# Kernel optimization log

Measured on AMD Instinct MI355X. Metric: run time of the kernel, lower is better.

## Reference

```python
import jax, jax.numpy as jnp
import numpy as np
from jax import lax

HEADS = 4
SR = 4
LN_EPS = 1e-5


def setup_inputs() -> dict:
    key = jax.random.key(0)
    ks = jax.random.split(key, 8)
    B, N, C = 8, 4096, 256
    w_scale = 0.05  # keep attention logits in a sane range
    return {
        "x": jax.random.normal(ks[0], (B, N, C), jnp.float32),
        "h": 64,
        "w": 64,
        "Wq": jax.random.normal(ks[1], (C, C), jnp.float32) * w_scale,
        "Wkv": jax.random.normal(ks[2], (C, 2 * C), jnp.float32) * w_scale,
        "sr_w": jax.random.normal(ks[3], (C, C, SR, SR), jnp.float32) * w_scale,
        "sr_b": jnp.zeros((C,), jnp.float32),
        "ln_g": jnp.ones((C,), jnp.float32),
        "ln_b": jnp.zeros((C,), jnp.float32),
        "Wo": jax.random.normal(ks[4], (C, C), jnp.float32) * w_scale,
        "bo": jnp.zeros((C,), jnp.float32),
    }


def _layernorm(x, g, b):
    mu = x.mean(-1, keepdims=True)
    var = ((x - mu) ** 2).mean(-1, keepdims=True)
    return (x - mu) * lax.rsqrt(var + LN_EPS) * g + b


def reference(x, h, w, Wq, Wkv, sr_w, sr_b, ln_g, ln_b, Wo, bo):
    B, N, C = x.shape
    hd = C // HEADS
    scale = hd ** -0.5
    # Q projection -> [B, H, N, hd]
    q = (x @ Wq).reshape(B, N, HEADS, hd).transpose(0, 2, 1, 3)
    # spatial reduction of K/V tokens: strided conv + LayerNorm
    x_kv = x.transpose(0, 2, 1).reshape(B, C, h, w)  # b (h w) c -> b c h w
    x_kv = lax.conv_general_dilated(
        x_kv, sr_w, window_strides=(SR, SR), padding="VALID",
        dimension_numbers=("NCHW", "OIHW", "NCHW"))
    x_kv = x_kv + sr_b[None, :, None, None]
    Nk = (h // SR) * (w // SR)
    x_kv = x_kv.reshape(B, C, Nk).transpose(0, 2, 1)  # b c h w -> b (h w) c
    x_kv = _layernorm(x_kv, ln_g, ln_b)
    # KV projection -> k, v each [B, H, Nk, hd]
    kv = (x_kv @ Wkv).reshape(B, Nk, 2, HEADS, hd)
    k = kv[:, :, 0].transpose(0, 2, 1, 3)
    v = kv[:, :, 1].transpose(0, 2, 1, 3)
    # attention: full [B, H, N, Nk] score matrix, softmax over kv axis
    att = jax.nn.softmax(jnp.einsum("bhxd,bhyd->bhxy", q, k) * scale, axis=-1)
    out = jnp.einsum("bhxy,bhyd->bhxd", att, v)
    out = out.transpose(0, 2, 1, 3).reshape(B, N, C)  # b h l d -> b l (h d)
    return out @ Wo + bo
```

## Files before the change

kernel.cpp:

```cpp
#include <hip/hip_runtime.h>

typedef __bf16 bf16;
typedef bf16 bf16x8 __attribute__((ext_vector_type(8)));
typedef bf16 bf16x4 __attribute__((ext_vector_type(4)));
typedef float f32x4 __attribute__((ext_vector_type(4)));

#define MFMA16(a, b, c) __builtin_amdgcn_mfma_f32_16x16x32_bf16(a, b, c, 0, 0, 0)

__device__ __forceinline__ void gload_lds16(const bf16* g, bf16* l) {
  __builtin_amdgcn_global_load_lds(
      (const __attribute__((address_space(1))) void*)g,
      (__attribute__((address_space(3))) void*)l, 16, 0, 0);
}

__global__ void k_prep(const float* __restrict__ x, const float* __restrict__ Wq,
                       const float* __restrict__ Wkv, const float* __restrict__ Wo,
                       const float* __restrict__ srw,
                       bf16* __restrict__ x_bf, bf16* __restrict__ WqT,
                       bf16* __restrict__ WkvT, bf16* __restrict__ WoT,
                       bf16* __restrict__ srwT) {
  int bid = blockIdx.x, tid = threadIdx.x;
  if (bid < 8192) {
    int i = (bid * 256 + tid) * 4;
    float4 v = *(const float4*)(x + i);
    bf16x4 o;
    o[0] = (bf16)v.x; o[1] = (bf16)v.y; o[2] = (bf16)v.z; o[3] = (bf16)v.w;
    *(bf16x4*)(x_bf + i) = o;
  } else if (bid < 9216) {
    int id = (bid - 8192) * 256 + tid;
    if (id < 65536) {
      int c = id >> 8, r = id & 255;
      WqT[c * 256 + (r ^ ((c & 7) << 3))] = (bf16)Wq[r * 256 + c];
    } else if (id < 196608) {
      int l = id - 65536;
      int c = l >> 8, r = l & 255;
      WkvT[l] = (bf16)Wkv[r * 512 + c];
    } else {
      int l = id - 196608;
      int c = l >> 8, r = l & 255;
      WoT[l] = (bf16)Wo[r * 256 + c];
    }
  } else {
    int id4 = ((bid - 9216) * 256 + tid) * 4;
    int o = id4 >> 12, rem = id4 & 4095;
    int i = rem >> 4, p = rem & 15;
    float4 v = *(const float4*)(srw + id4);
    srwT[(o << 12) + ((p + 0) << 8) + i] = (bf16)v.x;
    srwT[(o << 12) + ((p + 1) << 8) + i] = (bf16)v.y;
    srwT[(o << 12) + ((p + 2) << 8) + i] = (bf16)v.z;
    srwT[(o << 12) + ((p + 3) << 8) + i] = (bf16)v.w;
  }
}

template <int AMODE, int EMODE>
__global__ __launch_bounds__(256, 2) void k_gemm(
    const bf16* __restrict__ A, const bf16* __restrict__ Bt,
    void* __restrict__ Cout, const float* __restrict__ bias,
    int M, int N, int K) {
  constexpr int LDT = 72;
  __shared__ alignas(16) bf16 As[64 * LDT];
  __shared__ alignas(16) bf16 Bs[64 * LDT];
  int tid = threadIdx.x;
  int m0 = blockIdx.x * 64, n0 = blockIdx.y * 64;
  int kbeg = blockIdx.z * K;
  int wave = tid >> 6, lane = tid & 63;
  int quad = lane >> 4, l16 = lane & 15;

  f32x4 acc[4];
#pragma unroll
  for (int i = 0; i < 4; i++) acc[i] = (f32x4){0.f, 0.f, 0.f, 0.f};

  for (int k0 = kbeg; k0 < kbeg + K; k0 += 64) {
#pragma unroll
    for (int t = 0; t < 2; t++) {
      int c = tid + t * 256;
      int row = c >> 3, c8 = (c & 7) * 8;
      *(bf16x8*)&As[row * LDT + c8] =
          *(const bf16x8*)(A + (size_t)(m0 + row) * K + k0 + c8);
      *(bf16x8*)&Bs[row * LDT + c8] =
          *(const bf16x8*)(Bt + (size_t)(n0 + row) * K + k0 + c8);
    }
    __syncthreads();
#pragma unroll
    for (int kk = 0; kk < 64; kk += 32) {
      bf16x8 af = *(const bf16x8*)&As[(wave * 16 + l16) * LDT + kk + quad * 8];
#pragma unroll
      for (int nt = 0; nt < 4; nt++) {
        bf16x8 bfr = *(const bf16x8*)&Bs[(nt * 16 + l16) * LDT + kk + quad * 8];
        acc[nt] = MFMA16(af, bfr, acc[nt]);
      }
    }
    __syncthreads();
  }

  int rbase = m0 + wave * 16 + quad * 4;
#pragma unroll
  for (int nt = 0; nt < 4; nt++) {
    int col = n0 + nt * 16 + l16;
#pragma unroll
    for (int r = 0; r < 4; r++) {
      float v = acc[nt][r];
      int row = rbase + r;
      if constexpr (EMODE == 2) {
        int b = row >> 8, key = row & 255;
        int isv = col >> 8, c2 = col & 255;
        int hh = c2 >> 6, d = c2 & 63;
        int bh = b * 4 + hh;
        bf16* dst = (bf16*)Cout;
        if (isv == 0)
          dst[(((size_t)bh) * 256 + key) * 64 + (d ^ ((key & 7) << 3))] = (bf16)v;
        else
          dst[32 * 256 * 64 + (((size_t)bh) * 64 + d) * 256 + (key ^ ((d & 7) << 3))] = (bf16)v;
      } else {
        ((float*)Cout)[(size_t)row * N + col] = v + bias[col];
      }
    }
  }
}

template <int AMODE, int EMODE>
__global__ __launch_bounds__(256, 2) void k_gemm128(
    const bf16* __restrict__ A, const bf16* __restrict__ Bt,
    void* __restrict__ Cout, const float* __restrict__ bias,
    int M, int N, int K) {
  __shared__ alignas(16) bf16 As[128 * 64];
  __shared__ alignas(16) bf16 Bs[128 * 64];
  int tid = threadIdx.x;
  int m0 = blockIdx.x * 128, n0 = blockIdx.y * 128;
  int kbeg = blockIdx.z * K;
  int wave = tid >> 6, lane = tid & 63;
  int quad = lane >> 4, l16 = lane & 15;
  int wr = wave >> 1, wc = wave & 1;

  f32x4 acc[4][4];
#pragma unroll
  for (int i = 0; i < 4; i++)
#pragma unroll
    for (int j = 0; j < 4; j++) acc[i][j] = (f32x4){0.f, 0.f, 0.f, 0.f};

  for (int k0 = kbeg; k0 < kbeg + K; k0 += 64) {
#pragma unroll
    for (int t = 0; t < 4; t++) {
      int chunk = wave * 4 + t;
      int row = chunk * 8 + (lane >> 3);
      int c8 = (lane & 7) * 8;
      const bf16* asrc;
      if constexpr (AMODE == 0) {
        asrc = A + (size_t)(m0 + row) * K + k0 + c8;
      } else {
        int m = m0 + row;
        int b = m >> 8, tt = m & 255;
        int oh = tt >> 4, ow = tt & 15;
        int p = k0 >> 8;
        int kh = p >> 2, kw = p & 3;
        int tok = (oh * 4 + kh) * 64 + ow * 4 + kw;
        asrc = A + ((size_t)(b * 4096 + tok) << 8) + (k0 & 255) + c8;
      }
      gload_lds16(asrc, As + chunk * 512);
      gload_lds16(Bt + (size_t)(n0 + row) * ((AMODE == 1) ? 4096 : K) + k0 + c8,
                  Bs + chunk * 512);
    }
    __syncthreads();
#pragma unroll
    for (int kk = 0; kk < 64; kk += 32) {
      bf16x8 af[4], bfr[4];
#pragma unroll
      for (int mt = 0; mt < 4; mt++)
        af[mt] = *(const bf16x8*)&As[(wr * 64 + mt * 16 + l16) * 64 + kk + quad * 8];
#pragma unroll
      for (int nt = 0; nt < 4; nt++)
        bfr[nt] = *(const bf16x8*)&Bs[(wc * 64 + nt * 16 + l16) * 64 + kk + quad * 8];
#pragma unroll
      for (int mt = 0; mt < 4; mt++)
#pragma unroll
        for (int nt = 0; nt < 4; nt++)
          acc[mt][nt] = MFMA16(af[mt], bfr[nt], acc[mt][nt]);
    }
    __syncthreads();
  }

#pragma unroll
  for (int mt = 0; mt < 4; mt++) {
    int rbase = m0 + wr * 64 + mt * 16 + quad * 4;
#pragma unroll
    for (int nt = 0; nt < 4; nt++) {
      int col = n0 + wc * 64 + nt * 16 + l16;
#pragma unroll
      for (int r = 0; r < 4; r++) {
        float v = acc[mt][nt][r];
        int row = rbase + r;
        if constexpr (EMODE == 3) {
          ((float*)Cout)[(size_t)row * N + col] = v + bias[col];
        } else {
          ((float*)Cout)[((size_t)blockIdx.z * M + row) * N + col] = v;
        }
      }
    }
  }
}

__global__ void k_ln(const float* __restrict__ part, const float* __restrict__ srb,
                     const float* __restrict__ g, const float* __restrict__ bb,
                     bf16* __restrict__ out) {
  int row = blockIdx.x * 4 + (threadIdx.x >> 6);
  int lane = threadIdx.x & 63;
  size_t off = (size_t)row * 256 + lane * 4;
  float4 v = *(const float4*)&part[off];
#pragma unroll
  for (int z = 1; z < 8; z++) {
    float4 p = *(const float4*)&part[(size_t)z * 2048 * 256 + off];
    v.x += p.x; v.y += p.y; v.z += p.z; v.w += p.w;
  }
  int c = lane * 4;
  v.x += srb[c + 0]; v.y += srb[c + 1]; v.z += srb[c + 2]; v.w += srb[c + 3];
  float s = v.x + v.y + v.z + v.w;
#pragma unroll
  for (int i = 1; i < 64; i <<= 1) s += __shfl_xor(s, i, 64);
  float mu = s * (1.f / 256.f);
  float d0 = v.x - mu, d1 = v.y - mu, d2 = v.z - mu, d3 = v.w - mu;
  float q = d0 * d0 + d1 * d1 + d2 * d2 + d3 * d3;
#pragma unroll
  for (int i = 1; i < 64; i <<= 1) q += __shfl_xor(q, i, 64);
  float rs = rsqrtf(q * (1.f / 256.f) + 1e-5f);
  bf16x4 o;
  o[0] = (bf16)(d0 * rs * g[c + 0] + bb[c + 0]);
  o[1] = (bf16)(d1 * rs * g[c + 1] + bb[c + 1]);
  o[2] = (bf16)(d2 * rs * g[c + 2] + bb[c + 2]);
  o[3] = (bf16)(d3 * rs * g[c + 3] + bb[c + 3]);
  *(bf16x4*)&out[(size_t)row * 256 + c] = o;
}

__global__ __launch_bounds__(256, 3) void k_attn(
    const bf16* __restrict__ xbf,
    const bf16* __restrict__ WqT,
    const bf16* __restrict__ Kg,
    const bf16* __restrict__ Vg,
    bf16* __restrict__ O) {
  int bh = blockIdx.x, qt = blockIdx.y;
  int b = bh >> 2, h = bh & 3;
  int tid = threadIdx.x, wave = tid >> 6, lane = tid & 63;
  int quad = lane >> 4, l16 = lane & 15;

  __shared__ alignas(16) bf16 smem[24576];
  bf16* R0  = smem;
  bf16* R2a = smem + 16384;
  bf16* R2b = smem + 20480;

  const bf16* Kbh = Kg + ((size_t)bh << 14);
  const bf16* Vbh = Vg + ((size_t)bh << 14);
  const bf16* Wqh = WqT + ((size_t)(h * 64) << 8);

#pragma unroll
  for (int t = 0; t < 8; t++) {
    int chunk = t * 4 + wave;
    gload_lds16(Wqh + chunk * 512 + lane * 8, R0 + chunk * 512);
  }
#pragma unroll
  for (int t = 0; t < 2; t++) {
    int chunk = wave * 2 + t;
    gload_lds16(Vbh + (chunk * 8 + (lane >> 3)) * 256 + 0 + (lane & 7) * 8,
                R2a + chunk * 512);
  }
  const bf16* xrow =
      xbf + (((size_t)(b * 4096 + qt * 64 + wave * 16 + l16)) << 8) + quad * 8;
  bf16x8 ax[8];
#pragma unroll
  for (int j = 0; j < 8; j++) ax[j] = *(const bf16x8*)(xrow + j * 32);

  __syncthreads();

  f32x4 q[4];
#pragma unroll
  for (int i = 0; i < 4; i++) q[i] = (f32x4){0.f, 0.f, 0.f, 0.f};
#pragma unroll
  for (int j = 0; j < 8; j++) {
#pragma unroll
    for (int nt = 0; nt < 4; nt++) {
      int wrow = nt * 16 + l16;
      bf16x8 bw = *(const bf16x8*)&R0[wrow * 256 +
                                      ((j * 32 + quad * 8) ^ ((wrow & 7) << 3))];
      q[nt] = MFMA16(ax[j], bw, q[nt]);
    }
  }
  __syncthreads();

#pragma unroll
  for (int nt = 0; nt < 4; nt++)
#pragma unroll
    for (int r = 0; r < 4; r++) {
      int qr = wave * 16 + quad * 4 + r;
      R2b[qr * 64 + ((nt * 16 + l16) ^ ((qr & 7) << 3))] = (bf16)q[nt][r];
    }
#pragma unroll
  for (int t = 0; t < 8; t++) {
    int chunk = t * 4 + wave;
    gload_lds16(Kbh + chunk * 512 + lane * 8, R0 + chunk * 512);
  }
  __syncthreads();

  int arow = wave * 16 + l16;
  int asw = (arow & 7) << 3;
  bf16x8 aq0 = *(const bf16x8*)&R2b[arow * 64 + ((quad * 8) ^ asw)];
  bf16x8 aq1 = *(const bf16x8*)&R2b[arow * 64 + ((32 + quad * 8) ^ asw)];
  asm volatile("s_waitcnt lgkmcnt(0)" ::: "memory");
#pragma unroll
  for (int t = 0; t < 2; t++) {
    int chunk = wave * 2 + t;
    gload_lds16(Vbh + (chunk * 8 + (lane >> 3)) * 256 + 64 + (lane & 7) * 8,
                R2b + chunk * 512);
  }

  f32x4 s[16];
#pragma unroll
  for (int i = 0; i < 16; i++) s[i] = (f32x4){0.f, 0.f, 0.f, 0.f};
#pragma unroll
  for (int nt = 0; nt < 16; nt++) {
    int krow = nt * 16 + l16;
    const bf16* kb = R0 + krow * 64;
    int sw = (krow & 7) << 3;
    bf16x8 b0 = *(const bf16x8*)(kb + ((quad * 8) ^ sw));
    bf16x8 b1 = *(const bf16x8*)(kb + ((32 + quad * 8) ^ sw));
    s[nt] = MFMA16(aq0, b0, s[nt]);
    s[nt] = MFMA16(aq1, b1, s[nt]);
  }

  const float scale = 0.125f;
#pragma unroll
  for (int r = 0; r < 4; r++) {
    float m = -1e30f;
#pragma unroll
    for (int nt = 0; nt < 16; nt++) m = fmaxf(m, s[nt][r]);
#pragma unroll
    for (int i = 1; i < 16; i <<= 1) m = fmaxf(m, __shfl_xor(m, i, 64));
    float sum = 0.f;
#pragma unroll
    for (int nt = 0; nt < 16; nt++) {
      float e = __expf((s[nt][r] - m) * scale);
      s[nt][r] = e;
      sum += e;
    }
#pragma unroll
    for (int i = 1; i < 16; i <<= 1) sum += __shfl_xor(sum, i, 64);
    float inv = 1.f / sum;
#pragma unroll
    for (int nt = 0; nt < 16; nt++) s[nt][r] *= inv;
  }

  __syncthreads();

#pragma unroll
  for (int nt = 0; nt < 16; nt++)
#pragma unroll
    for (int r = 0; r < 4; r++) {
      int prow = wave * 16 + quad * 4 + r;
      R0[prow * 256 + ((nt * 16 + l16) ^ ((prow & 7) << 3))] = (bf16)s[nt][r];
    }

  const bf16* pb = R0 + arow * 256;
  f32x4 o[4];
#pragma unroll
  for (int i = 0; i < 4; i++) o[i] = (f32x4){0.f, 0.f, 0.f, 0.f};

#pragma unroll
  for (int cq = 0; cq < 4; cq++) {
    const bf16* Vbuf = (cq & 1) ? R2b : R2a;
#pragma unroll
    for (int k0 = 0; k0 < 64; k0 += 32) {
      bf16x8 ap = *(const bf16x8*)(pb + ((cq * 64 + k0 + quad * 8) ^ asw));
#pragma unroll
      for (int nt = 0; nt < 4; nt++) {
        int vrow = nt * 16 + l16;
        bf16x8 bv = *(const bf16x8*)&Vbuf[vrow * 64 +
                                          ((k0 + quad * 8) ^ ((vrow & 7) << 3))];
        o[nt] = MFMA16(ap, bv, o[nt]);
      }
    }
    if (cq < 3) {
      __syncthreads();
      if (cq < 2) {
        bf16* nb = (cq & 1) ? R2b : R2a;
#pragma unroll
        for (int t = 0; t < 2; t++) {
          int chunk = wave * 2 + t;
          gload_lds16(Vbh + (chunk * 8 + (lane >> 3)) * 256 + (cq + 2) * 64 +
                          (lane & 7) * 8,
                      nb + chunk * 512);
        }
      }
    }
  }

  size_t orow = (size_t)b * 4096 + qt * 64 + wave * 16 + quad * 4;
#pragma unroll
  for (int nt = 0; nt < 4; nt++) {
    int col = h * 64 + nt * 16 + l16;
#pragma unroll
    for (int r = 0; r < 4; r++) O[(orow + r) * 256 + col] = (bf16)o[nt][r];
  }
}

extern "C" void kernel_launch(void* const* d_in, const int* in_sizes, int n_in,
                              void* d_out, int out_size, void* d_ws, size_t ws_size,
                              hipStream_t stream) {
  (void)in_sizes; (void)n_in; (void)out_size; (void)ws_size;
  const float* x   = (const float*)d_in[0];
  const float* Wq  = (const float*)d_in[3];
  const float* Wkv = (const float*)d_in[4];
  const float* srw = (const float*)d_in[5];
  const float* srb = (const float*)d_in[6];
  const float* lng = (const float*)d_in[7];
  const float* lnb = (const float*)d_in[8];
  const float* Wo  = (const float*)d_in[9];
  const float* bo  = (const float*)d_in[10];
  float* out = (float*)d_out;

  char* ws = (char*)d_ws;
  bf16*  x_bf  = (bf16*)(ws + 0);
  bf16*  AObuf = (bf16*)(ws + 16777216);
  float* convp = (float*)(ws + 33554432);
  bf16*  WqT   = (bf16*)(ws + 50331648);
  bf16*  WkvT  = (bf16*)(ws + 50462720);
  bf16*  WoT   = (bf16*)(ws + 50724864);
  bf16*  srwT  = (bf16*)(ws + 50855936);
  bf16*  xln   = (bf16*)(ws + 52953088);
  bf16*  kvbuf = (bf16*)(ws + 54001664);

  k_prep<<<10240, 256, 0, stream>>>(x, Wq, Wkv, Wo, srw, x_bf, WqT, WkvT, WoT, srwT);
  k_gemm128<1, 4><<<dim3(16, 2, 8), 256, 0, stream>>>(x_bf, srwT, convp, nullptr, 2048, 256, 512);
  k_ln<<<512, 256, 0, stream>>>(convp, srb, lng, lnb, xln);
  k_gemm<0, 2><<<dim3(32, 8), 256, 0, stream>>>(xln, WkvT, kvbuf, nullptr, 2048, 512, 256);
  k_attn<<<dim3(32, 64), 256, 0, stream>>>(x_bf, WqT, kvbuf, kvbuf + (size_t)32 * 256 * 64, AObuf);
  k_gemm128<0, 3><<<dim3(256, 2), 256, 0, stream>>>(AObuf, WoT, out, bo, 32768, 256, 256);
}
```

Measured before the change: 177.0 us.

## Fuse output projection into attention kernel and loop over all heads per block

Each attention block now processes one 64-row query tile across all four heads, keeping per-head outputs in registers. It then applies the Wo projection and bias in-kernel, writing fp32 output directly. This removes the bf16 intermediate attention-output buffer round trip and the separate output GEMM launch. Wo is pre-swizzled in prep to match the LDS layout. The trade-off is that the grid drops from 2048 to 512 blocks, each doing serialized per-head work with more barriers, lower occupancy (launch bound 3 to 2) and higher register pressure.

```diff
diff --git a/kernel.cpp b/kernel.cpp
--- a/kernel.cpp
+++ b/kernel.cpp
@@ -38,7 +38,7 @@
     } else {
       int l = id - 196608;
       int c = l >> 8, r = l & 255;
-      WoT[l] = (bf16)Wo[r * 256 + c];
+      WoT[c * 256 + (r ^ ((c & 7) << 3))] = (bf16)Wo[r * 256 + c];
     }
   } else {
     int id4 = ((bid - 9216) * 256 + tid) * 4;
@@ -230,172 +230,196 @@
   *(bf16x4*)&out[(size_t)row * 256 + c] = o;
 }
 
-__global__ __launch_bounds__(256, 3) void k_attn(
+__global__ __launch_bounds__(256, 2) void k_attn_mega(
     const bf16* __restrict__ xbf,
     const bf16* __restrict__ WqT,
     const bf16* __restrict__ Kg,
     const bf16* __restrict__ Vg,
-    bf16* __restrict__ O) {
-  int bh = blockIdx.x, qt = blockIdx.y;
-  int b = bh >> 2, h = bh & 3;
+    const bf16* __restrict__ WoT,
+    const float* __restrict__ bo,
+    float* __restrict__ out) {
+  int b = blockIdx.x, qt = blockIdx.y;
   int tid = threadIdx.x, wave = tid >> 6, lane = tid & 63;
   int quad = lane >> 4, l16 = lane & 15;
 
-  __shared__ alignas(16) bf16 smem[24576];
-  bf16* R0  = smem;
-  bf16* R2a = smem + 16384;
-  bf16* R2b = smem + 20480;
-
-  const bf16* Kbh = Kg + ((size_t)bh << 14);
-  const bf16* Vbh = Vg + ((size_t)bh << 14);
-  const bf16* Wqh = WqT + ((size_t)(h * 64) << 8);
-
-#pragma unroll
-  for (int t = 0; t < 8; t++) {
-    int chunk = t * 4 + wave;
-    gload_lds16(Wqh + chunk * 512 + lane * 8, R0 + chunk * 512);
-  }
-#pragma unroll
-  for (int t = 0; t < 2; t++) {
-    int chunk = wave * 2 + t;
-    gload_lds16(Vbh + (chunk * 8 + (lane >> 3)) * 256 + 0 + (lane & 7) * 8,
-                R2a + chunk * 512);
-  }
-  const bf16* xrow =
-      xbf + (((size_t)(b * 4096 + qt * 64 + wave * 16 + l16)) << 8) + quad * 8;
-  bf16x8 ax[8];
-#pragma unroll
-  for (int j = 0; j < 8; j++) ax[j] = *(const bf16x8*)(xrow + j * 32);
-
-  __syncthreads();
-
-  f32x4 q[4];
-#pragma unroll
-  for (int i = 0; i < 4; i++) q[i] = (f32x4){0.f, 0.f, 0.f, 0.f};
-#pragma unroll
-  for (int j = 0; j < 8; j++) {
-#pragma unroll
-    for (int nt = 0; nt < 4; nt++) {
-      int wrow = nt * 16 + l16;
-      bf16x8 bw = *(const bf16x8*)&R0[wrow * 256 +
-                                      ((j * 32 + quad * 8) ^ ((wrow & 7) << 3))];
-      q[nt] = MFMA16(ax[j], bw, q[nt]);
-    }
-  }
-  __syncthreads();
-
-#pragma unroll
-  for (int nt = 0; nt < 4; nt++)
-#pragma unroll
-    for (int r = 0; r < 4; r++) {
-      int qr = wave * 16 + quad * 4 + r;
-      R2b[qr * 64 + ((nt * 16 + l16) ^ ((qr & 7) << 3))] = (bf16)q[nt][r];
-    }
-#pragma unroll
-  for (int t = 0; t < 8; t++) {
-    int chunk = t * 4 + wave;
-    gload_lds16(Kbh + chunk * 512 + lane * 8, R0 + chunk * 512);
-  }
-  __syncthreads();
+  __shared__ alignas(16) bf16 smem[36864];
+  bf16* R0 = smem;
+  bf16* RV = smem + 16384;
+  bf16* RQ = smem + 32768;
 
   int arow = wave * 16 + l16;
   int asw = (arow & 7) << 3;
-  bf16x8 aq0 = *(const bf16x8*)&R2b[arow * 64 + ((quad * 8) ^ asw)];
-  bf16x8 aq1 = *(const bf16x8*)&R2b[arow * 64 + ((32 + quad * 8) ^ asw)];
-  asm volatile("s_waitcnt lgkmcnt(0)" ::: "memory");
-#pragma unroll
-  for (int t = 0; t < 2; t++) {
-    int chunk = wave * 2 + t;
-    gload_lds16(Vbh + (chunk * 8 + (lane >> 3)) * 256 + 64 + (lane & 7) * 8,
-                R2b + chunk * 512);
-  }
-
-  f32x4 s[16];
-#pragma unroll
-  for (int i = 0; i < 16; i++) s[i] = (f32x4){0.f, 0.f, 0.f, 0.f};
-#pragma unroll
-  for (int nt = 0; nt < 16; nt++) {
-    int krow = nt * 16 + l16;
-    const bf16* kb = R0 + krow * 64;
-    int sw = (krow & 7) << 3;
-    bf16x8 b0 = *(const bf16x8*)(kb + ((quad * 8) ^ sw));
-    bf16x8 b1 = *(const bf16x8*)(kb + ((32 + quad * 8) ^ sw));
-    s[nt] = MFMA16(aq0, b0, s[nt]);
-    s[nt] = MFMA16(aq1, b1, s[nt]);
-  }
-
-  const float scale = 0.125f;
-#pragma unroll
-  for (int r = 0; r < 4; r++) {
-    float m = -1e30f;
-#pragma unroll
-    for (int nt = 0; nt < 16; nt++) m = fmaxf(m, s[nt][r]);
-#pragma unroll
-    for (int i = 1; i < 16; i <<= 1) m = fmaxf(m, __shfl_xor(m, i, 64));
-    float sum = 0.f;
+
+  const bf16* xrow =
+      xbf + (((size_t)(b * 4096 + qt * 64 + arow)) << 8) + quad * 8;
+  bf16x8 ax[8];
+#pragma unroll
+  for (int j = 0; j < 8; j++) ax[j] = *(const bf16x8*)(xrow + j * 32);
+
+  f32x4 o_all[4][4];
+
+#pragma unroll
+  for (int h = 0; h < 4; h++) {
+    int bh = b * 4 + h;
+    const bf16* Wqh = WqT + ((size_t)(h * 64) << 8);
+    const bf16* Kbh = Kg + ((size_t)bh << 14);
+    const bf16* Vbh = Vg + ((size_t)bh << 14);
+
+#pragma unroll
+    for (int t = 0; t < 8; t++) {
+      int chunk = t * 4 + wave;
+      gload_lds16(Wqh + chunk * 512 + lane * 8, R0 + chunk * 512);
+    }
+    __syncthreads();
+
+#pragma unroll
+    for (int t = 0; t < 8; t++) {
+      int chunk = t * 4 + wave;
+      gload_lds16(Vbh + chunk * 512 + lane * 8, RV + chunk * 512);
+    }
+
+    f32x4 q[4];
+#pragma unroll
+    for (int i = 0; i < 4; i++) q[i] = (f32x4){0.f, 0.f, 0.f, 0.f};
+#pragma unroll
+    for (int j = 0; j < 8; j++) {
+#pragma unroll
+      for (int nt = 0; nt < 4; nt++) {
+        int wrow = nt * 16 + l16;
+        bf16x8 bw = *(const bf16x8*)&R0[wrow * 256 +
+                                        ((j * 32 + quad * 8) ^ ((wrow & 7) << 3))];
+        q[nt] = MFMA16(ax[j], bw, q[nt]);
+      }
+    }
+    __syncthreads();
+
+#pragma unroll
+    for (int nt = 0; nt < 4; nt++)
+#pragma unroll
+      for (int r = 0; r < 4; r++) {
+        int qr = wave * 16 + quad * 4 + r;
+        RQ[qr * 64 + ((nt * 16 + l16) ^ ((qr & 7) << 3))] = (bf16)q[nt][r];
+      }
+#pragma unroll
+    for (int t = 0; t < 8; t++) {
+      int chunk = t * 4 + wave;
+      gload_lds16(Kbh + chunk * 512 + lane * 8, R0 + chunk * 512);
+    }
+    __syncthreads();
+
+    bf16x8 aq0 = *(const bf16x8*)&RQ[arow * 64 + ((quad * 8) ^ asw)];
+    bf16x8 aq1 = *(const bf16x8*)&RQ[arow * 64 + ((32 + quad * 8) ^ asw)];
+
+    f32x4 s[16];
+#pragma unroll
+    for (int i = 0; i < 16; i++) s[i] = (f32x4){0.f, 0.f, 0.f, 0.f};
 #pragma unroll
     for (int nt = 0; nt < 16; nt++) {
-      float e = __expf((s[nt][r] - m) * scale);
-      s[nt][r] = e;
-      sum += e;
-    }
-#pragma unroll
-    for (int i = 1; i < 16; i <<= 1) sum += __shfl_xor(sum, i, 64);
-    float inv = 1.f / sum;
-#pragma unroll
-    for (int nt = 0; nt < 16; nt++) s[nt][r] *= inv;
-  }
-
-  __syncthreads();
-
-#pragma unroll
-  for (int nt = 0; nt < 16; nt++)
+      int krow = nt * 16 + l16;
+      const bf16* kb = R0 + krow * 64;
+      int sw = (krow & 7) << 3;
+      bf16x8 b0 = *(const bf16x8*)(kb + ((quad * 8) ^ sw));
+      bf16x8 b1 = *(const bf16x8*)(kb + ((32 + quad * 8) ^ sw));
+      s[nt] = MFMA16(aq0, b0, s[nt]);
+      s[nt] = MFMA16(aq1, b1, s[nt]);
+    }
+
+    const float scale = 0.125f;
 #pragma unroll
     for (int r = 0; r < 4; r++) {
-      int prow = wave * 16 + quad * 4 + r;
-      R0[prow * 256 + ((nt * 16 + l16) ^ ((prow & 7) << 3))] = (bf16)s[nt][r];
-    }
-
-  const bf16* pb = R0 + arow * 256;
-  f32x4 o[4];
-#pragma unroll
-  for (int i = 0; i < 4; i++) o[i] = (f32x4){0.f, 0.f, 0.f, 0.f};
-
-#pragma unroll
-  for (int cq = 0; cq < 4; cq++) {
-    const bf16* Vbuf = (cq & 1) ? R2b : R2a;
-#pragma unroll
-    for (int k0 = 0; k0 < 64; k0 += 32) {
-      bf16x8 ap = *(const bf16x8*)(pb + ((cq * 64 + k0 + quad * 8) ^ asw));
+      float m = -1e30f;
+#pragma unroll
+      for (int nt = 0; nt < 16; nt++) m = fmaxf(m, s[nt][r]);
+#pragma unroll
+      for (int i = 1; i < 16; i <<= 1) m = fmaxf(m, __shfl_xor(m, i, 64));
+      float sum = 0.f;
+#pragma unroll
+      for (int nt = 0; nt < 16; nt++) {
+        float e = __expf((s[nt][r] - m) * scale);
+        s[nt][r] = e;
+        sum += e;
+      }
+#pragma unroll
+      for (int i = 1; i < 16; i <<= 1) sum += __shfl_xor(sum, i, 64);
+      float inv = 1.f / sum;
+#pragma unroll
+      for (int nt = 0; nt < 16; nt++) s[nt][r] *= inv;
+    }
+
+    __syncthreads();
+
+#pragma unroll
+    for (int nt = 0; nt < 16; nt++)
+#pragma unroll
+      for (int r = 0; r < 4; r++) {
+        int prow = wave * 16 + quad * 4 + r;
+        R0[prow * 256 + ((nt * 16 + l16) ^ ((prow & 7) << 3))] = (bf16)s[nt][r];
+      }
+
+    const bf16* pb = R0 + arow * 256;
+#pragma unroll
+    for (int nt = 0; nt < 4; nt++) o_all[h][nt] = (f32x4){0.f, 0.f, 0.f, 0.f};
+#pragma unroll
+    for (int k0 = 0; k0 < 256; k0 += 32) {
+      bf16x8 ap = *(const bf16x8*)(pb + ((k0 + quad * 8) ^ asw));
 #pragma unroll
       for (int nt = 0; nt < 4; nt++) {
         int vrow = nt * 16 + l16;
-        bf16x8 bv = *(const bf16x8*)&Vbuf[vrow * 64 +
-                                          ((k0 + quad * 8) ^ ((vrow & 7) << 3))];
-        o[nt] = MFMA16(ap, bv, o[nt]);
-      }
-    }
-    if (cq < 3) {
-      __syncthreads();
-      if (cq < 2) {
-        bf16* nb = (cq & 1) ? R2b : R2a;
-#pragma unroll
-        for (int t = 0; t < 2; t++) {
-          int chunk = wave * 2 + t;
-          gload_lds16(Vbh + (chunk * 8 + (lane >> 3)) * 256 + (cq + 2) * 64 +
-                          (lane & 7) * 8,
-                      nb + chunk * 512);
-        }
-      }
-    }
-  }
-
-  size_t orow = (size_t)b * 4096 + qt * 64 + wave * 16 + quad * 4;
-#pragma unroll
-  for (int nt = 0; nt < 4; nt++) {
-    int col = h * 64 + nt * 16 + l16;
-#pragma unroll
-    for (int r = 0; r < 4; r++) O[(orow + r) * 256 + col] = (bf16)o[nt][r];
+        bf16x8 bv = *(const bf16x8*)&RV[vrow * 256 +
+                                        ((k0 + quad * 8) ^ ((vrow & 7) << 3))];
+        o_all[h][nt] = MFMA16(ap, bv, o_all[h][nt]);
+      }
+    }
+    __syncthreads();
+  }
+
+#pragma unroll
+  for (int h = 0; h < 4; h++)
+#pragma unroll
+    for (int nt = 0; nt < 4; nt++)
+#pragma unroll
+      for (int r = 0; r < 4; r++) {
+        int orow = wave * 16 + quad * 4 + r;
+        int col = h * 64 + nt * 16 + l16;
+        R0[orow * 256 + (col ^ ((orow & 7) << 3))] = (bf16)o_all[h][nt][r];
+      }
+  bf16x8 oa[8];
+#pragma unroll
+  for (int j = 0; j < 8; j++)
+    oa[j] = *(const bf16x8*)&R0[arow * 256 + ((j * 32 + quad * 8) ^ asw)];
+
+  size_t orow0 = (size_t)b * 4096 + qt * 64 + wave * 16 + quad * 4;
+#pragma unroll
+  for (int c = 0; c < 4; c++) {
+#pragma unroll
+    for (int t = 0; t < 8; t++) {
+      int chunk = t * 4 + wave;
+      gload_lds16(WoT + (((size_t)c * 64) << 8) + chunk * 512 + lane * 8,
+                  RV + chunk * 512);
+    }
+    __syncthreads();
+
+    f32x4 oo[4];
+#pragma unroll
+    for (int i = 0; i < 4; i++) oo[i] = (f32x4){0.f, 0.f, 0.f, 0.f};
+#pragma unroll
+    for (int j = 0; j < 8; j++) {
+#pragma unroll
+      for (int nt = 0; nt < 4; nt++) {
+        int wrow = nt * 16 + l16;
+        bf16x8 bw = *(const bf16x8*)&RV[wrow * 256 +
+                                        ((j * 32 + quad * 8) ^ ((wrow & 7) << 3))];
+        oo[nt] = MFMA16(oa[j], bw, oo[nt]);
+      }
+    }
+#pragma unroll
+    for (int nt = 0; nt < 4; nt++) {
+      int col = c * 64 + nt * 16 + l16;
+#pragma unroll
+      for (int r = 0; r < 4; r++)
+        out[(orow0 + r) * 256 + col] = oo[nt][r] + bo[col];
+    }
+    if (c < 3) __syncthreads();
   }
 }
 
@@ -416,19 +440,18 @@
 
   char* ws = (char*)d_ws;
   bf16*  x_bf  = (bf16*)(ws + 0);
-  bf16*  AObuf = (bf16*)(ws + 16777216);
-  float* convp = (float*)(ws + 33554432);
-  bf16*  WqT   = (bf16*)(ws + 50331648);
-  bf16*  WkvT  = (bf16*)(ws + 50462720);
-  bf16*  WoT   = (bf16*)(ws + 50724864);
-  bf16*  srwT  = (bf16*)(ws + 50855936);
-  bf16*  xln   = (bf16*)(ws + 52953088);
-  bf16*  kvbuf = (bf16*)(ws + 54001664);
+  float* convp = (float*)(ws + 16777216);
+  bf16*  WqT   = (bf16*)(ws + 33554432);
+  bf16*  WkvT  = (bf16*)(ws + 33685504);
+  bf16*  WoT   = (bf16*)(ws + 33947648);
+  bf16*  srwT  = (bf16*)(ws + 34078720);
+  bf16*  xln   = (bf16*)(ws + 36175872);
+  bf16*  kvbuf = (bf16*)(ws + 37224448);
 
   k_prep<<<10240, 256, 0, stream>>>(x, Wq, Wkv, Wo, srw, x_bf, WqT, WkvT, WoT, srwT);
   k_gemm128<1, 4><<<dim3(16, 2, 8), 256, 0, stream>>>(x_bf, srwT, convp, nullptr, 2048, 256, 512);
   k_ln<<<512, 256, 0, stream>>>(convp, srb, lng, lnb, xln);
   k_gemm<0, 2><<<dim3(32, 8), 256, 0, stream>>>(xln, WkvT, kvbuf, nullptr, 2048, 512, 256);
-  k_attn<<<dim3(32, 64), 256, 0, stream>>>(x_bf, WqT, kvbuf, kvbuf + (size_t)32 * 256 * 64, AObuf);
-  k_gemm128<0, 3><<<dim3(256, 2), 256, 0, stream>>>(AObuf, WoT, out, bo, 32768, 256, 256);
-}
+  k_attn_mega<<<dim3(8, 64), 256, 0, stream>>>(
+      x_bf, WqT, kvbuf, kvbuf + (size_t)32 * 256 * 64, WoT, bo, out);
+}
```

After: 180.5 us. No clear change (+2.0%).

## Add dedicated 64-row output projection GEMM and raise MFMA priority in attention

Applied to the files above, without the earlier changes.

Replaces the generic 128-tile output projection GEMM with a specialized kernel where each block computes 64 rows by the full 256 output columns. Each wave owns 64 columns and the A tile is shared by all waves, giving 512 blocks for better CU fill, with the bias add fused into the store. It also wraps the MFMA loops in the attention kernel with s_setprio so waves issuing matrix math get scheduling priority over waves doing loads. The new GEMM uses unswizzled LDS reads and reloads the full 256-row weight tile in every block, which may cause bank conflicts and extra memory traffic.

```diff
diff --git a/kernel.cpp b/kernel.cpp
--- a/kernel.cpp
+++ b/kernel.cpp
@@ -199,6 +199,69 @@
   }
 }
 
+__global__ __launch_bounds__(256, 3) void k_gemm_out(
+    const bf16* __restrict__ A, const bf16* __restrict__ Bt,
+    float* __restrict__ out, const float* __restrict__ bias) {
+  __shared__ alignas(16) bf16 As[64 * 64];
+  __shared__ alignas(16) bf16 Bs[256 * 64];
+  int tid = threadIdx.x;
+  int m0 = blockIdx.x * 64;
+  int wave = tid >> 6, lane = tid & 63;
+  int quad = lane >> 4, l16 = lane & 15;
+
+  f32x4 acc[4][4];
+#pragma unroll
+  for (int i = 0; i < 4; i++)
+#pragma unroll
+    for (int j = 0; j < 4; j++) acc[i][j] = (f32x4){0.f, 0.f, 0.f, 0.f};
+
+  for (int k0 = 0; k0 < 256; k0 += 64) {
+    int c8 = (lane & 7) * 8;
+#pragma unroll
+    for (int t = 0; t < 2; t++) {
+      int chunk = wave * 2 + t;
+      int row = chunk * 8 + (lane >> 3);
+      gload_lds16(A + (size_t)(m0 + row) * 256 + k0 + c8, As + chunk * 512);
+    }
+#pragma unroll
+    for (int t = 0; t < 8; t++) {
+      int chunk = wave * 8 + t;
+      int row = chunk * 8 + (lane >> 3);
+      gload_lds16(Bt + (size_t)row * 256 + k0 + c8, Bs + chunk * 512);
+    }
+    __syncthreads();
+#pragma unroll
+    for (int kk = 0; kk < 64; kk += 32) {
+      bf16x8 af[4], bfr[4];
+#pragma unroll
+      for (int mt = 0; mt < 4; mt++)
+        af[mt] = *(const bf16x8*)&As[(mt * 16 + l16) * 64 + kk + quad * 8];
+#pragma unroll
+      for (int nt = 0; nt < 4; nt++)
+        bfr[nt] = *(const bf16x8*)&Bs[(wave * 64 + nt * 16 + l16) * 64 + kk + quad * 8];
+#pragma unroll
+      for (int mt = 0; mt < 4; mt++)
+#pragma unroll
+        for (int nt = 0; nt < 4; nt++)
+          acc[mt][nt] = MFMA16(af[mt], bfr[nt], acc[mt][nt]);
+    }
+    __syncthreads();
+  }
+
+#pragma unroll
+  for (int mt = 0; mt < 4; mt++) {
+    int rbase = m0 + mt * 16 + quad * 4;
+#pragma unroll
+    for (int nt = 0; nt < 4; nt++) {
+      int col = wave * 64 + nt * 16 + l16;
+      float bb = bias[col];
+#pragma unroll
+      for (int r = 0; r < 4; r++)
+        out[(size_t)(rbase + r) * 256 + col] = acc[mt][nt][r] + bb;
+    }
+  }
+}
+
 __global__ void k_ln(const float* __restrict__ part, const float* __restrict__ srb,
                      const float* __restrict__ g, const float* __restrict__ bb,
                      bf16* __restrict__ out) {
@@ -272,6 +335,7 @@
   f32x4 q[4];
 #pragma unroll
   for (int i = 0; i < 4; i++) q[i] = (f32x4){0.f, 0.f, 0.f, 0.f};
+  __builtin_amdgcn_s_setprio(1);
 #pragma unroll
   for (int j = 0; j < 8; j++) {
 #pragma unroll
@@ -282,6 +346,7 @@
       q[nt] = MFMA16(ax[j], bw, q[nt]);
     }
   }
+  __builtin_amdgcn_s_setprio(0);
   __syncthreads();
 
 #pragma unroll
@@ -313,6 +378,7 @@
   f32x4 s[16];
 #pragma unroll
   for (int i = 0; i < 16; i++) s[i] = (f32x4){0.f, 0.f, 0.f, 0.f};
+  __builtin_amdgcn_s_setprio(1);
 #pragma unroll
   for (int nt = 0; nt < 16; nt++) {
     int krow = nt * 16 + l16;
@@ -323,6 +389,7 @@
     s[nt] = MFMA16(aq0, b0, s[nt]);
     s[nt] = MFMA16(aq1, b1, s[nt]);
   }
+  __builtin_amdgcn_s_setprio(0);
 
   const float scale = 0.125f;
 #pragma unroll
@@ -364,6 +431,7 @@
 #pragma unroll
   for (int cq = 0; cq < 4; cq++) {
     const bf16* Vbuf = (cq & 1) ? R2b : R2a;
+    __builtin_amdgcn_s_setprio(1);
 #pragma unroll
     for (int k0 = 0; k0 < 64; k0 += 32) {
       bf16x8 ap = *(const bf16x8*)(pb + ((cq * 64 + k0 + quad * 8) ^ asw));
@@ -375,6 +443,7 @@
         o[nt] = MFMA16(ap, bv, o[nt]);
       }
     }
+    __builtin_amdgcn_s_setprio(0);
     if (cq < 3) {
       __syncthreads();
       if (cq < 2) {
@@ -430,5 +499,5 @@
   k_ln<<<512, 256, 0, stream>>>(convp, srb, lng, lnb, xln);
   k_gemm<0, 2><<<dim3(32, 8), 256, 0, stream>>>(xln, WkvT, kvbuf, nullptr, 2048, 512, 256);
   k_attn<<<dim3(32, 64), 256, 0, stream>>>(x_bf, WqT, kvbuf, kvbuf + (size_t)32 * 256 * 64, AObuf);
-  k_gemm128<0, 3><<<dim3(256, 2), 256, 0, stream>>>(AObuf, WoT, out, bo, 32768, 256, 256);
-}
+  k_gemm_out<<<512, 256, 0, stream>>>(AObuf, WoT, out, bo);
+}
```

Result: no change. 176.0 us (-0.5%).
